# Performance work log

Hardware: AMD Instinct MI355X
Metric: run time of the kernel (lower is better)

## Reference

```python
import jax, jax.numpy as jnp
import numpy as np

B, T, L = 64, 1024, 256


def setup_inputs() -> dict:
    key = jax.random.key(0)
    k1, k2, k3, k4, k5 = jax.random.split(key, 5)
    return {
        "h": jax.random.normal(k1, (B, T, L), jnp.float32),
        "labels": jax.random.randint(k2, (B, T), 0, L),
        "mask": jnp.ones((B, T), dtype=bool),
        "trans_matrix": jax.random.normal(k3, (L, L), jnp.float32) * 0.1,
        "start_trans": jax.random.normal(k4, (L,), jnp.float32) * 0.1,
        "end_trans": jax.random.normal(k5, (L,), jnp.float32) * 0.1,
    }


def _crf_log_likelihood(h, labels, mask, trans, start, end):
    # h: [B,T,L], labels: [B,T] int, mask: [B,T] bool
    Bn, Tn, Ln = h.shape
    maskf = mask.astype(h.dtype)
    ar = jnp.arange(Bn)

    # ---- numerator (score of the gold path) ----
    y_t = labels[:, :-1]          # [B,T-1]
    y_t1 = labels[:, 1:]          # [B,T-1]
    emit = jnp.take_along_axis(h[:, :-1], y_t[..., None], axis=2)[..., 0]  # [B,T-1]
    tr = trans[y_t, y_t1]         # [B,T-1]
    num = start[labels[:, 0]] + jnp.sum(emit * maskf[:, :-1] + tr * maskf[:, 1:], axis=1)
    last_idx = jnp.sum(mask.astype(jnp.int32), axis=1) - 1  # [B]
    last_labels = labels[ar, last_idx]
    num = num + h[ar, -1, last_labels] * maskf[:, -1] + end[last_labels]

    # ---- denominator (log partition, forward algorithm via scan) ----
    def step(score, inp):
        h_t, m_t = inp  # [B,L], [B] bool
        # score[b,i] + trans[i,j] + h_t[b,j] -> logsumexp over i
        s = jax.nn.logsumexp(score[:, :, None] + trans[None, :, :] + h_t[:, None, :], axis=1)
        score = jnp.where(m_t[:, None], s, score)
        return score, None

    init = start[None, :] + h[:, 0]  # [B,L]
    h_seq = jnp.swapaxes(h, 0, 1)[1:]       # [T-1,B,L]
    m_seq = jnp.swapaxes(mask, 0, 1)[1:]    # [T-1,B]
    final, _ = jax.lax.scan(step, init, (h_seq, m_seq))
    denom = jax.nn.logsumexp(final + end[None, :], axis=1)  # [B]

    return num - denom


def reference(h, labels, mask, trans_matrix, start_trans, end_trans):
    return _crf_log_likelihood(h, labels, mask, trans_matrix, start_trans, end_trans)
```

## Files before the change

kernel.cpp:

```cpp
#include <hip/hip_runtime.h>
#include <math.h>

#define NB 64
#define NT 1024
#define NL 256

typedef __attribute__((ext_vector_type(8))) short bf16x8;
typedef __attribute__((ext_vector_type(4))) float f32x4;

__device__ __forceinline__ unsigned short f32_bf16u(float f) {
    unsigned u = __float_as_uint(f);
    u += 0x7FFFu + ((u >> 16) & 1u);
    return (unsigned short)(u >> 16);
}

__global__ __launch_bounds__(256) void num_kernel(
    const float* __restrict__ h, const int* __restrict__ labels,
    const float* __restrict__ trans, const float* __restrict__ start,
    const float* __restrict__ end, float* __restrict__ num_out)
{
    int b = blockIdx.x;
    int tid = threadIdx.x;
    const int* lab = labels + b * NT;
    const float* hb = h + (size_t)b * NT * NL;

    float acc = 0.f;
    int t0 = tid * 4;
    #pragma unroll
    for (int k = 0; k < 4; ++k) {
        int t = t0 + k;
        if (t < NT - 1) {
            int yt  = lab[t];
            int yt1 = lab[t + 1];
            acc += hb[t * NL + yt] + trans[yt * NL + yt1];
        }
    }
    #pragma unroll
    for (int o = 32; o > 0; o >>= 1) acc += __shfl_xor(acc, o);
    __shared__ float red[4];
    if ((tid & 63) == 0) red[tid >> 6] = acc;
    __syncthreads();
    if (tid == 0) {
        float s = red[0] + red[1] + red[2] + red[3];
        int y0 = lab[0], yl = lab[NT - 1];
        s += start[y0] + hb[(NT - 1) * NL + yl] + end[yl];
        num_out[b] = s;
    }
}


#define FOR8(M) M(0) M(1) M(2) M(3) M(4) M(5) M(6) M(7)

#define DECL_B0(f) bf16x8 b0_##f;
#define DECL_B1(f) bf16x8 b1_##f;
#define LOAD_B(tt, f) { \
    const float* tp = trans + (size_t)((f) * 32 + l4 * 8) * NL + cb + (tt) * 16; \
    bf16x8 tmp; \
    tmp[0] = (short)f32_bf16u(__expf(tp[0 * NL])); tmp[1] = (short)f32_bf16u(__expf(tp[1 * NL])); \
    tmp[2] = (short)f32_bf16u(__expf(tp[2 * NL])); tmp[3] = (short)f32_bf16u(__expf(tp[3 * NL])); \
    tmp[4] = (short)f32_bf16u(__expf(tp[4 * NL])); tmp[5] = (short)f32_bf16u(__expf(tp[5 * NL])); \
    tmp[6] = (short)f32_bf16u(__expf(tp[6 * NL])); tmp[7] = (short)f32_bf16u(__expf(tp[7 * NL])); \
    b##tt##_##f = tmp; }
#define LOAD_B0(f) LOAD_B(0, f)
#define LOAD_B1(f) LOAD_B(1, f)
#define PIN_B0(f) asm volatile("" : "+a"(b0_##f));
#define PIN_B1(f) asm volatile("" : "+a"(b1_##f));

#define MFMA_B(Creg, areg, bvar) \
    Creg = __builtin_amdgcn_mfma_f32_16x16x32_bf16(areg, bvar, Creg, 0, 0, 0);

#define LDA(f) (*(const bf16x8*)(pb + (f) * 64))

__global__ __launch_bounds__(512)
__attribute__((amdgpu_waves_per_eu(2, 2)))
void fwd_kernel(
    const float* __restrict__ h, const float* __restrict__ trans,
    const float* __restrict__ start, const float* __restrict__ end,
    const float* __restrict__ num_in, float* __restrict__ out)
{
    int b = blockIdx.x;
    int tid = threadIdx.x;
    int wv = tid >> 6;
    int lane = tid & 63;
    int l4 = lane >> 4;
    int lc = lane & 15;
    int cb = wv * 32 + lc;

    const float* hb = h + (size_t)b * NT * NL;

    FOR8(DECL_B0) FOR8(DECL_B1)
    FOR8(LOAD_B0) FOR8(LOAD_B1)
    FOR8(PIN_B0)  FOR8(PIN_B1)

    __shared__ __align__(16) unsigned short p2[2][NL];
    __shared__ int klds[2];
    __shared__ float zred[8];

    if (tid < NL) {
        float q0 = __expf(start[tid] + hb[tid]);
        p2[0][tid] = f32_bf16u(q0);
        if (tid == 0) klds[0] = ilogbf(q0);
    }
    float ehva0 = __expf(hb[NL + cb]),     ehvb0 = __expf(hb[NL + cb + 16]);
    float hva1  = hb[2 * NL + cb],         hvb1  = hb[2 * NL + cb + 16];
    __syncthreads();

    int Ksum = 0;
    float qa = 0.f, qb = 0.f;

    for (int t = 1; t < NT; ++t) {
        int kcur = klds[(t - 1) & 1];
        float scale = __int_as_float((127 - kcur) << 23);
        float hva2 = 0.f, hvb2 = 0.f;
        if (t + 2 < NT) {
            size_t o = (size_t)(t + 2) * NL;
            hva2 = hb[o + cb]; hvb2 = hb[o + cb + 16];
        }
        float ehva1 = __expf(hva1), ehvb1 = __expf(hvb1);

        const char* pb = (const char*)&p2[(t - 1) & 1][0] + (l4 << 4);
        bf16x8 a0 = LDA(0); bf16x8 a1 = LDA(1); bf16x8 a2 = LDA(2); bf16x8 a3 = LDA(3);
        bf16x8 a4 = LDA(4); bf16x8 a5 = LDA(5); bf16x8 a6 = LDA(6); bf16x8 a7 = LDA(7);

        f32x4 C0a = {0.f,0.f,0.f,0.f}, C1a = {0.f,0.f,0.f,0.f};
        f32x4 C2a = {0.f,0.f,0.f,0.f}, C3a = {0.f,0.f,0.f,0.f};
        f32x4 C0b = {0.f,0.f,0.f,0.f}, C1b = {0.f,0.f,0.f,0.f};
        f32x4 C2b = {0.f,0.f,0.f,0.f}, C3b = {0.f,0.f,0.f,0.f};

        MFMA_B(C0a, a0, b0_0)  MFMA_B(C0b, a0, b1_0)
        MFMA_B(C1a, a1, b0_1)  MFMA_B(C1b, a1, b1_1)
        MFMA_B(C2a, a2, b0_2)  MFMA_B(C2b, a2, b1_2)
        MFMA_B(C3a, a3, b0_3)  MFMA_B(C3b, a3, b1_3)
        MFMA_B(C0a, a4, b0_4)  MFMA_B(C0b, a4, b1_4)
        MFMA_B(C1a, a5, b0_5)  MFMA_B(C1b, a5, b1_5)
        MFMA_B(C2a, a6, b0_6)  MFMA_B(C2b, a6, b1_6)
        MFMA_B(C3a, a7, b0_7)  MFMA_B(C3b, a7, b1_7)

        float sa = (C0a[0] + C1a[0]) + (C2a[0] + C3a[0]);
        float sb = (C0b[0] + C1b[0]) + (C2b[0] + C3b[0]);

        qa = sa * scale * ehva0;
        qb = sb * scale * ehvb0;

        unsigned short* pn = &p2[t & 1][0];
        if (l4 == 0) {
            pn[cb]      = f32_bf16u(qa);
            pn[cb + 16] = f32_bf16u(qb);
        }
        if (tid == 0) { klds[t & 1] = ilogbf(qa); Ksum += kcur; }

        ehva0 = ehva1; ehvb0 = ehvb1;
        hva1 = hva2;   hvb1 = hvb2;
        __syncthreads();
    }

    float r = 0.f;
    if (l4 == 0) r = qa * __expf(end[cb]) + qb * __expf(end[cb + 16]);
    #pragma unroll
    for (int o = 32; o > 0; o >>= 1) r += __shfl_xor(r, o);
    if (lane == 0) zred[wv] = r;
    __syncthreads();
    if (tid == 0) {
        float Zf = 0.f;
        #pragma unroll
        for (int i = 0; i < 8; ++i) Zf += zred[i];
        float denom = __logf(Zf) + (float)Ksum * 0.69314718056f;
        out[b] = num_in[b] - denom;
    }
}

extern "C" void kernel_launch(void* const* d_in, const int* in_sizes, int n_in,
                              void* d_out, int out_size, void* d_ws, size_t ws_size,
                              hipStream_t stream)
{
    const float* h      = (const float*)d_in[0];
    const int*   labels = (const int*)d_in[1];
    const float* trans  = (const float*)d_in[3];
    const float* start  = (const float*)d_in[4];
    const float* end    = (const float*)d_in[5];
    float* out    = (float*)d_out;
    float* num_ws = (float*)d_ws;

    num_kernel<<<NB, 256, 0, stream>>>(h, labels, trans, start, end, num_ws);
    fwd_kernel<<<NB, 512, 0, stream>>>(h, trans, start, end, num_ws, out);
}
```

Before: 542.7 us.

## Split forward recurrence contraction across K-halves with LDS partial-sum reduction

Repartitions the per-step matrix-vector product so each of the 8 waves handles half of the reduction dimension (128 rows) and 64 output columns, instead of all 256 rows for 32 columns. This shortens each wave's serial MFMA chain from 8-deep to 4-deep dependent accumulations per output tile and lets A loads interleave with MFMAs. The two K-half partial sums are combined through an LDS buffer, which adds a second barrier per timestep and a serial epilogue phase run by 256 threads.

Measured after the change: 565.3 us. 4.2% more time.

```diff
diff --git a/kernel.cpp b/kernel.cpp
--- a/kernel.cpp
+++ b/kernel.cpp
@@ -49,27 +49,26 @@
 }
 
 
-#define FOR8(M) M(0) M(1) M(2) M(3) M(4) M(5) M(6) M(7)
+#define FOR4(M) M(0) M(1) M(2) M(3)
 
-#define DECL_B0(f) bf16x8 b0_##f;
-#define DECL_B1(f) bf16x8 b1_##f;
-#define LOAD_B(tt, f) { \
-    const float* tp = trans + (size_t)((f) * 32 + l4 * 8) * NL + cb + (tt) * 16; \
+#define DECL_BT(tt) bf16x8 b##tt##_0, b##tt##_1, b##tt##_2, b##tt##_3;
+
+#define LOAD_B1(tt, f) { \
+    const float* tp = trans + (size_t)(kh * 128 + (f) * 32 + l4 * 8) * NL \
+                      + tq * 64 + (tt) * 16 + lc; \
     bf16x8 tmp; \
     tmp[0] = (short)f32_bf16u(__expf(tp[0 * NL])); tmp[1] = (short)f32_bf16u(__expf(tp[1 * NL])); \
     tmp[2] = (short)f32_bf16u(__expf(tp[2 * NL])); tmp[3] = (short)f32_bf16u(__expf(tp[3 * NL])); \
     tmp[4] = (short)f32_bf16u(__expf(tp[4 * NL])); tmp[5] = (short)f32_bf16u(__expf(tp[5 * NL])); \
     tmp[6] = (short)f32_bf16u(__expf(tp[6 * NL])); tmp[7] = (short)f32_bf16u(__expf(tp[7 * NL])); \
     b##tt##_##f = tmp; }
-#define LOAD_B0(f) LOAD_B(0, f)
-#define LOAD_B1(f) LOAD_B(1, f)
-#define PIN_B0(f) asm volatile("" : "+a"(b0_##f));
-#define PIN_B1(f) asm volatile("" : "+a"(b1_##f));
+#define LOAD_BT(tt) LOAD_B1(tt,0) LOAD_B1(tt,1) LOAD_B1(tt,2) LOAD_B1(tt,3)
+
+#define PIN_BT(tt) asm volatile("" : \
+    "+a"(b##tt##_0), "+a"(b##tt##_1), "+a"(b##tt##_2), "+a"(b##tt##_3));
 
 #define MFMA_B(Creg, areg, bvar) \
     Creg = __builtin_amdgcn_mfma_f32_16x16x32_bf16(areg, bvar, Creg, 0, 0, 0);
-
-#define LDA(f) (*(const bf16x8*)(pb + (f) * 64))
 
 __global__ __launch_bounds__(512)
 __attribute__((amdgpu_waves_per_eu(2, 2)))
@@ -80,90 +79,89 @@
 {
     int b = blockIdx.x;
     int tid = threadIdx.x;
-    int wv = tid >> 6;
+    int w = tid >> 6;
+    int kh = w >> 2;
+    int tq = w & 3;
     int lane = tid & 63;
     int l4 = lane >> 4;
     int lc = lane & 15;
-    int cb = wv * 32 + lc;
 
     const float* hb = h + (size_t)b * NT * NL;
 
-    FOR8(DECL_B0) FOR8(DECL_B1)
-    FOR8(LOAD_B0) FOR8(LOAD_B1)
-    FOR8(PIN_B0)  FOR8(PIN_B1)
+    FOR4(DECL_BT)
+    FOR4(LOAD_BT)
+    FOR4(PIN_BT)
 
     __shared__ __align__(16) unsigned short p2[2][NL];
+    __shared__ __align__(8) float sparts[NL][2];
     __shared__ int klds[2];
-    __shared__ float zred[8];
+    __shared__ float zred[4];
 
+    float qlast = 0.f, hv0 = 0.f, hv1 = 0.f;
     if (tid < NL) {
         float q0 = __expf(start[tid] + hb[tid]);
         p2[0][tid] = f32_bf16u(q0);
         if (tid == 0) klds[0] = ilogbf(q0);
+        qlast = q0;
+        hv0 = hb[NL + tid];
+        hv1 = hb[2 * NL + tid];
     }
-    float ehva0 = __expf(hb[NL + cb]),     ehvb0 = __expf(hb[NL + cb + 16]);
-    float hva1  = hb[2 * NL + cb],         hvb1  = hb[2 * NL + cb + 16];
     __syncthreads();
 
     int Ksum = 0;
-    float qa = 0.f, qb = 0.f;
+    float* spw = &sparts[tq * 64 + l4 * 16 + lc][kh];
 
     for (int t = 1; t < NT; ++t) {
         int kcur = klds[(t - 1) & 1];
-        float scale = __int_as_float((127 - kcur) << 23);
-        float hva2 = 0.f, hvb2 = 0.f;
-        if (t + 2 < NT) {
-            size_t o = (size_t)(t + 2) * NL;
-            hva2 = hb[o + cb]; hvb2 = hb[o + cb + 16];
+        float hv2 = 0.f;
+        if (tid < NL && t + 2 < NT) hv2 = hb[(size_t)(t + 2) * NL + tid];
+
+        const char* pAc = (const char*)&p2[(t - 1) & 1][0] + kh * 256 + (l4 << 4);
+        f32x4 C0 = {0.f,0.f,0.f,0.f}, C1 = {0.f,0.f,0.f,0.f};
+        f32x4 C2 = {0.f,0.f,0.f,0.f}, C3 = {0.f,0.f,0.f,0.f};
+
+        bf16x8 a0 = *(const bf16x8*)(pAc + 0);
+        bf16x8 a1 = *(const bf16x8*)(pAc + 64);
+        MFMA_B(C0, a0, b0_0)  MFMA_B(C1, a0, b1_0)
+        MFMA_B(C2, a0, b2_0)  MFMA_B(C3, a0, b3_0)
+        bf16x8 a2 = *(const bf16x8*)(pAc + 128);
+        MFMA_B(C0, a1, b0_1)  MFMA_B(C1, a1, b1_1)
+        MFMA_B(C2, a1, b2_1)  MFMA_B(C3, a1, b3_1)
+        bf16x8 a3 = *(const bf16x8*)(pAc + 192);
+        MFMA_B(C0, a2, b0_2)  MFMA_B(C1, a2, b1_2)
+        MFMA_B(C2, a2, b2_2)  MFMA_B(C3, a2, b3_2)
+        MFMA_B(C0, a3, b0_3)  MFMA_B(C1, a3, b1_3)
+        MFMA_B(C2, a3, b2_3)  MFMA_B(C3, a3, b3_3)
+
+        float pv = (l4 < 2) ? ((l4 == 0) ? C0[0] : C1[0])
+                            : ((l4 == 2) ? C2[0] : C3[0]);
+        *spw = pv;
+        __syncthreads();
+
+        if (tid < NL) {
+            float2 pp = *(const float2*)&sparts[tid][0];
+            float s = pp.x + pp.y;
+            float scale = __int_as_float((127 - kcur) << 23);
+            float q = s * scale * __expf(hv0);
+            p2[t & 1][tid] = f32_bf16u(q);
+            if (tid == 0) { klds[t & 1] = ilogbf(q); Ksum += kcur; }
+            qlast = q;
+            hv0 = hv1;
+            hv1 = hv2;
         }
-        float ehva1 = __expf(hva1), ehvb1 = __expf(hvb1);
-
-        const char* pb = (const char*)&p2[(t - 1) & 1][0] + (l4 << 4);
-        bf16x8 a0 = LDA(0); bf16x8 a1 = LDA(1); bf16x8 a2 = LDA(2); bf16x8 a3 = LDA(3);
-        bf16x8 a4 = LDA(4); bf16x8 a5 = LDA(5); bf16x8 a6 = LDA(6); bf16x8 a7 = LDA(7);
-
-        f32x4 C0a = {0.f,0.f,0.f,0.f}, C1a = {0.f,0.f,0.f,0.f};
-        f32x4 C2a = {0.f,0.f,0.f,0.f}, C3a = {0.f,0.f,0.f,0.f};
-        f32x4 C0b = {0.f,0.f,0.f,0.f}, C1b = {0.f,0.f,0.f,0.f};
-        f32x4 C2b = {0.f,0.f,0.f,0.f}, C3b = {0.f,0.f,0.f,0.f};
-
-        MFMA_B(C0a, a0, b0_0)  MFMA_B(C0b, a0, b1_0)
-        MFMA_B(C1a, a1, b0_1)  MFMA_B(C1b, a1, b1_1)
-        MFMA_B(C2a, a2, b0_2)  MFMA_B(C2b, a2, b1_2)
-        MFMA_B(C3a, a3, b0_3)  MFMA_B(C3b, a3, b1_3)
-        MFMA_B(C0a, a4, b0_4)  MFMA_B(C0b, a4, b1_4)
-        MFMA_B(C1a, a5, b0_5)  MFMA_B(C1b, a5, b1_5)
-        MFMA_B(C2a, a6, b0_6)  MFMA_B(C2b, a6, b1_6)
-        MFMA_B(C3a, a7, b0_7)  MFMA_B(C3b, a7, b1_7)
-
-        float sa = (C0a[0] + C1a[0]) + (C2a[0] + C3a[0]);
-        float sb = (C0b[0] + C1b[0]) + (C2b[0] + C3b[0]);
-
-        qa = sa * scale * ehva0;
-        qb = sb * scale * ehvb0;
-
-        unsigned short* pn = &p2[t & 1][0];
-        if (l4 == 0) {
-            pn[cb]      = f32_bf16u(qa);
-            pn[cb + 16] = f32_bf16u(qb);
-        }
-        if (tid == 0) { klds[t & 1] = ilogbf(qa); Ksum += kcur; }
-
-        ehva0 = ehva1; ehvb0 = ehvb1;
-        hva1 = hva2;   hvb1 = hvb2;
         __syncthreads();
     }
 
     float r = 0.f;
-    if (l4 == 0) r = qa * __expf(end[cb]) + qb * __expf(end[cb + 16]);
-    #pragma unroll
-    for (int o = 32; o > 0; o >>= 1) r += __shfl_xor(r, o);
-    if (lane == 0) zred[wv] = r;
+    if (tid < NL) {
+        r = qlast * __expf(end[tid]);
+        #pragma unroll
+        for (int o = 32; o > 0; o >>= 1) r += __shfl_xor(r, o);
+        if (lane == 0) zred[w] = r;
+    }
     __syncthreads();
     if (tid == 0) {
-        float Zf = 0.f;
-        #pragma unroll
-        for (int i = 0; i < 8; ++i) Zf += zred[i];
+        float Zf = (zred[0] + zred[1]) + (zred[2] + zred[3]);
         float denom = __logf(Zf) + (float)Ksum * 0.69314718056f;
         out[b] = num_in[b] - denom;
     }
```
